# Kernel tuning notes

Measured on AMD Instinct MI355X. Metric: run time of the kernel, lower is better.

## Reference

```python
import jax, jax.numpy as jnp
import numpy as np

EPS_F = 1e-6   # epsilon_F global in original repo
GAMMA = 0.8
K = 5
BN_EPS = 1e-5
M = 128
N = 100000
E = 1600000
MY = 10

def setup_inputs() -> dict:
    key = jax.random.key(0)
    ks = jax.random.split(key, 6)
    X = jax.random.normal(ks[0], (M, N), dtype=jnp.float32)
    # xavier_uniform for F: limit = sqrt(6/(m+m))
    lim = float(np.sqrt(6.0 / (M + M)))
    F_mat = jax.random.uniform(ks[1], (M, M), dtype=jnp.float32, minval=-lim, maxval=lim)
    B = (1.0 / np.sqrt(M)) * jax.random.normal(ks[2], (MY, M), dtype=jnp.float32)
    bn_weight = jnp.ones((M,), dtype=jnp.float32)
    bn_bias = jnp.zeros((M,), dtype=jnp.float32)
    edge_val = jax.random.uniform(ks[3], (E,), dtype=jnp.float32)
    edge_row = jax.random.randint(ks[4], (E,), 0, N, dtype=jnp.int64 if jax.config.jax_enable_x64 else jnp.int32)
    edge_col = jax.random.randint(ks[5], (E,), 0, N, dtype=jnp.int64 if jax.config.jax_enable_x64 else jnp.int32)
    return {"X": X, "F_mat": F_mat, "B": B, "bn_weight": bn_weight,
            "bn_bias": bn_bias, "edge_val": edge_val,
            "edge_row": edge_row, "edge_col": edge_col}

def reference(X, F_mat, B, bn_weight, bn_bias, edge_val, edge_row, edge_col):
    n = X.shape[1]
    # normalized Gram matrix g(F) = F^T F / (||F^T F||_fro + eps)
    FF = F_mat.T @ F_mat                       # [m, m]
    G = FF / (jnp.linalg.norm(FF) + EPS_F)
    X_first = X                                # [m, n]

    def step(Xc, _):
        Y = Xc.T                               # [n, m]
        # SpMM: (S_t @ Y)[r] += val * Y[c]
        SY = jax.ops.segment_sum(edge_val[:, None] * Y[edge_col], edge_row,
                                 num_segments=n)   # [n, m]
        Xn = GAMMA * (G @ SY.T) + X_first          # [m, n]
        return Xn, None

    Xk, _ = jax.lax.scan(step, X, None, length=K)
    out = Xk.T                                 # [n, m]
    # BatchNorm1d over feature dim (training-mode batch stats); dropout omitted (eval)
    mu = out.mean(axis=0)
    var = out.var(axis=0)
    out = (out - mu) * jax.lax.rsqrt(var + BN_EPS) * bn_weight + bn_bias
    return out @ B.T                           # [n, m_y]
```

## Files before the change

kernel.cpp:

```cpp
#include <hip/hip_runtime.h>
#include <math.h>

#define MDIM 128
#define MY 10
#define GAMMA 0.8f
#define KITER 5

__device__ __forceinline__ float bf2f(unsigned short h) {
    return __uint_as_float(((unsigned int)h) << 16);
}
__device__ __forceinline__ unsigned short f2bf(float f) {
    unsigned int u = __float_as_uint(f);
    u += 0x7fffu + ((u >> 16) & 1u);
    return (unsigned short)(u >> 16);
}

__global__ void k_transpose(const float* __restrict__ X, float* __restrict__ Y0,
                            unsigned short* __restrict__ Y0h, int n) {
    __shared__ float tile[32][33];
    int r0 = blockIdx.x * 32;
    int f0 = blockIdx.y * 32;
    int tx = threadIdx.x, ty = threadIdx.y;
    #pragma unroll
    for (int i = 0; i < 32; i += 8) {
        tile[ty + i][tx] = X[(size_t)(f0 + ty + i) * n + (r0 + tx)];
    }
    __syncthreads();
    #pragma unroll
    for (int i = 0; i < 32; i += 8) {
        float v = tile[tx][ty + i];
        Y0[(size_t)(r0 + ty + i) * MDIM + (f0 + tx)] = v;
        Y0h[(size_t)(r0 + ty + i) * MDIM + (f0 + tx)] = f2bf(v);
    }
}

__global__ void k_gram(const float* __restrict__ F, float* __restrict__ FF,
                       float* __restrict__ normAcc) {
    int i = blockIdx.x, j = threadIdx.x;
    float acc = 0.f;
    for (int k = 0; k < MDIM; ++k)
        acc = fmaf(F[k * MDIM + i], F[k * MDIM + j], acc);
    FF[i * MDIM + j] = acc;
    __shared__ float red[MDIM];
    red[j] = acc * acc;
    __syncthreads();
    for (int s = 64; s > 0; s >>= 1) {
        if (j < s) red[j] += red[j + s];
        __syncthreads();
    }
    if (j == 0) atomicAdd(normAcc, red[0]);
}

__global__ void k_gnorm(const float* __restrict__ FF, const float* __restrict__ normAcc,
                        float* __restrict__ G) {
    int idx = blockIdx.x * 256 + threadIdx.x;
    float s = GAMMA / (sqrtf(*normAcc) + 1e-6f);
    G[idx] = FF[idx] * s;
}

__global__ void k_hist(const int* __restrict__ erow, int* __restrict__ cnt, int E) {
    int e = blockIdx.x * 256 + threadIdx.x;
    if (e < E) atomicAdd(&cnt[erow[e]], 1);
}

__global__ void k_scan1(const int* __restrict__ cnt, int* __restrict__ blockSums, int n) {
    int tid = threadIdx.x;
    int base = blockIdx.x * 1024 + tid * 4;
    int s = 0;
    if (base + 3 < n) {
        int4 v = *(const int4*)&cnt[base];
        s = v.x + v.y + v.z + v.w;
    } else {
        for (int i = 0; i < 4; ++i)
            if (base + i < n) s += cnt[base + i];
    }
    __shared__ int red[256];
    red[tid] = s;
    __syncthreads();
    for (int st = 128; st > 0; st >>= 1) {
        if (tid < st) red[tid] += red[tid + st];
        __syncthreads();
    }
    if (tid == 0) blockSums[blockIdx.x] = red[0];
}

__global__ void k_scan2(int* __restrict__ blockSums, int* __restrict__ row_off,
                        int nb, int n) {
    __shared__ int s[256];
    int tid = threadIdx.x;
    int v = (tid < nb) ? blockSums[tid] : 0;
    s[tid] = v;
    __syncthreads();
    for (int off = 1; off < 256; off <<= 1) {
        int t = (tid >= off) ? s[tid - off] : 0;
        __syncthreads();
        s[tid] += t;
        __syncthreads();
    }
    if (tid < nb) blockSums[tid] = s[tid] - v;
    if (tid == 0) row_off[n] = s[255];
}

__global__ void k_scan3(const int* __restrict__ cnt, const int* __restrict__ blockOff,
                        int* __restrict__ row_off, int n) {
    int tid = threadIdx.x;
    int base = blockIdx.x * 1024 + tid * 4;
    int v[4];
    #pragma unroll
    for (int i = 0; i < 4; ++i) v[i] = (base + i < n) ? cnt[base + i] : 0;
    int local = v[0] + v[1] + v[2] + v[3];
    __shared__ int s[256];
    s[tid] = local;
    __syncthreads();
    for (int off = 1; off < 256; off <<= 1) {
        int t = (tid >= off) ? s[tid - off] : 0;
        __syncthreads();
        s[tid] += t;
        __syncthreads();
    }
    int excl = s[tid] - local + blockOff[blockIdx.x];
    #pragma unroll
    for (int i = 0; i < 4; ++i) {
        if (base + i < n) { row_off[base + i] = excl; excl += v[i]; }
    }
}

__global__ void k_scatter(const int* __restrict__ erow, const int* __restrict__ ecol,
                          const float* __restrict__ eval_, int* __restrict__ cursor,
                          int* __restrict__ csr_col, float* __restrict__ csr_val, int E) {
    int e = blockIdx.x * 256 + threadIdx.x;
    if (e < E) {
        int r = erow[e];
        int pos = atomicAdd(&cursor[r], 1);
        csr_col[pos] = ecol[e];
        csr_val[pos] = eval_[e];
    }
}

__global__ void __launch_bounds__(256) k_spmm(const unsigned short* __restrict__ Yh,
                                              const int* __restrict__ row_off,
                                              const int* __restrict__ csr_col,
                                              const float* __restrict__ csr_val,
                                              float* __restrict__ SY, int n) {
    int row = blockIdx.x * 8 + (threadIdx.x >> 5);
    int tx = threadIdx.x & 31;
    if (row >= n) return;
    int e0 = row_off[row], e1 = row_off[row + 1];
    float4 acc = make_float4(0.f, 0.f, 0.f, 0.f);
    int e = e0;
    for (; e + 4 <= e1; e += 4) {
        float v0 = csr_val[e + 0];
        float v1 = csr_val[e + 1];
        float v2 = csr_val[e + 2];
        float v3 = csr_val[e + 3];
        int c0 = csr_col[e + 0];
        int c1 = csr_col[e + 1];
        int c2 = csr_col[e + 2];
        int c3 = csr_col[e + 3];
        ushort4 h0 = *(const ushort4*)&Yh[(size_t)c0 * MDIM + tx * 4];
        ushort4 h1 = *(const ushort4*)&Yh[(size_t)c1 * MDIM + tx * 4];
        ushort4 h2 = *(const ushort4*)&Yh[(size_t)c2 * MDIM + tx * 4];
        ushort4 h3 = *(const ushort4*)&Yh[(size_t)c3 * MDIM + tx * 4];
        acc.x = fmaf(v0, bf2f(h0.x), acc.x);
        acc.y = fmaf(v0, bf2f(h0.y), acc.y);
        acc.z = fmaf(v0, bf2f(h0.z), acc.z);
        acc.w = fmaf(v0, bf2f(h0.w), acc.w);
        acc.x = fmaf(v1, bf2f(h1.x), acc.x);
        acc.y = fmaf(v1, bf2f(h1.y), acc.y);
        acc.z = fmaf(v1, bf2f(h1.z), acc.z);
        acc.w = fmaf(v1, bf2f(h1.w), acc.w);
        acc.x = fmaf(v2, bf2f(h2.x), acc.x);
        acc.y = fmaf(v2, bf2f(h2.y), acc.y);
        acc.z = fmaf(v2, bf2f(h2.z), acc.z);
        acc.w = fmaf(v2, bf2f(h2.w), acc.w);
        acc.x = fmaf(v3, bf2f(h3.x), acc.x);
        acc.y = fmaf(v3, bf2f(h3.y), acc.y);
        acc.z = fmaf(v3, bf2f(h3.z), acc.z);
        acc.w = fmaf(v3, bf2f(h3.w), acc.w);
    }
    for (; e < e1; ++e) {
        float v = csr_val[e];
        int c = csr_col[e];
        ushort4 h = *(const ushort4*)&Yh[(size_t)c * MDIM + tx * 4];
        acc.x = fmaf(v, bf2f(h.x), acc.x);
        acc.y = fmaf(v, bf2f(h.y), acc.y);
        acc.z = fmaf(v, bf2f(h.z), acc.z);
        acc.w = fmaf(v, bf2f(h.w), acc.w);
    }
    *(float4*)&SY[(size_t)row * MDIM + tx * 4] = acc;
}

__global__ void __launch_bounds__(256) k_gemm(const float* __restrict__ SY,
                                              const float* __restrict__ G,
                                              const float* __restrict__ Y0,
                                              float* __restrict__ Yout,
                                              unsigned short* __restrict__ Yhout,
                                              int writeH, int n) {
    __shared__ float sG[MDIM * MDIM];
    int tid = threadIdx.x;
    #pragma unroll
    for (int i = 0; i < 16; ++i) {
        int idx = (i * 256 + tid) * 4;
        *(float4*)&sG[idx] = *(const float4*)&G[idx];
    }
    __syncthreads();
    int tx = tid & 31, ty = tid >> 5;
    size_t r0 = (size_t)blockIdx.x * 32 + ty * 4;
    int f0 = tx * 4;
    float4 acc[4];
    #pragma unroll
    for (int i = 0; i < 4; ++i) acc[i] = make_float4(0.f, 0.f, 0.f, 0.f);
    for (int j = 0; j < MDIM; j += 4) {
        float4 g0 = *(const float4*)&sG[(j + 0) * MDIM + f0];
        float4 g1 = *(const float4*)&sG[(j + 1) * MDIM + f0];
        float4 g2 = *(const float4*)&sG[(j + 2) * MDIM + f0];
        float4 g3 = *(const float4*)&sG[(j + 3) * MDIM + f0];
        #pragma unroll
        for (int i = 0; i < 4; ++i) {
            float4 sr = *(const float4*)&SY[(r0 + i) * MDIM + j];
            acc[i].x = fmaf(sr.x, g0.x, acc[i].x);
            acc[i].y = fmaf(sr.x, g0.y, acc[i].y);
            acc[i].z = fmaf(sr.x, g0.z, acc[i].z);
            acc[i].w = fmaf(sr.x, g0.w, acc[i].w);
            acc[i].x = fmaf(sr.y, g1.x, acc[i].x);
            acc[i].y = fmaf(sr.y, g1.y, acc[i].y);
            acc[i].z = fmaf(sr.y, g1.z, acc[i].z);
            acc[i].w = fmaf(sr.y, g1.w, acc[i].w);
            acc[i].x = fmaf(sr.z, g2.x, acc[i].x);
            acc[i].y = fmaf(sr.z, g2.y, acc[i].y);
            acc[i].z = fmaf(sr.z, g2.z, acc[i].z);
            acc[i].w = fmaf(sr.z, g2.w, acc[i].w);
            acc[i].x = fmaf(sr.w, g3.x, acc[i].x);
            acc[i].y = fmaf(sr.w, g3.y, acc[i].y);
            acc[i].z = fmaf(sr.w, g3.z, acc[i].z);
            acc[i].w = fmaf(sr.w, g3.w, acc[i].w);
        }
    }
    #pragma unroll
    for (int i = 0; i < 4; ++i) {
        float4 y0 = *(const float4*)&Y0[(r0 + i) * MDIM + f0];
        float4 o;
        o.x = acc[i].x + y0.x;
        o.y = acc[i].y + y0.y;
        o.z = acc[i].z + y0.z;
        o.w = acc[i].w + y0.w;
        *(float4*)&Yout[(r0 + i) * MDIM + f0] = o;
        if (writeH) {
            ushort4 h;
            h.x = f2bf(o.x);
            h.y = f2bf(o.y);
            h.z = f2bf(o.z);
            h.w = f2bf(o.w);
            *(ushort4*)&Yhout[(r0 + i) * MDIM + f0] = h;
        }
    }
}

__global__ void k_bnstats(const float* __restrict__ Y, float* __restrict__ stats, int n) {
    int f = threadIdx.x;
    int chunk = (n + gridDim.x - 1) / gridDim.x;
    int rbeg = blockIdx.x * chunk;
    int rend = rbeg + chunk;
    if (rend > n) rend = n;
    float s = 0.f, sq = 0.f;
    for (int r = rbeg; r < rend; ++r) {
        float v = Y[(size_t)r * MDIM + f];
        s += v;
        sq = fmaf(v, v, sq);
    }
    atomicAdd(&stats[f], s);
    atomicAdd(&stats[MDIM + f], sq);
}

__global__ void k_finalize(const float* __restrict__ stats, const float* __restrict__ B,
                           const float* __restrict__ bnw, const float* __restrict__ bnb,
                           float* __restrict__ Bs, float* __restrict__ cvec, int n) {
    int f = threadIdx.x;
    float inv_n = 1.f / (float)n;
    float mu = stats[f] * inv_n;
    float var = stats[MDIM + f] * inv_n - mu * mu;
    float rs = rsqrtf(var + 1e-5f);
    float sw = rs * bnw[f];
    float cv = bnb[f] - mu * sw;
    __shared__ float red[MDIM];
    for (int o = 0; o < MY; ++o) {
        float b = B[o * MDIM + f];
        Bs[o * MDIM + f] = b * sw;
        red[f] = b * cv;
        __syncthreads();
        for (int s = 64; s > 0; s >>= 1) {
            if (f < s) red[f] += red[f + s];
            __syncthreads();
        }
        if (f == 0) cvec[o] = red[0];
        __syncthreads();
    }
}

__global__ void __launch_bounds__(256) k_project(const float* __restrict__ Y,
                                                 const float* __restrict__ Bs,
                                                 const float* __restrict__ cvec,
                                                 float* __restrict__ out, int n) {
    __shared__ float yt[16 * 129];
    __shared__ float sB[MY * 129];
    __shared__ float sc[MY];
    int tid = threadIdx.x;
    size_t rbase = (size_t)blockIdx.x * 16;
    for (int idx = tid; idx < 16 * MDIM; idx += 256) {
        int r = idx >> 7, f = idx & 127;
        yt[r * 129 + f] = Y[(rbase + r) * MDIM + f];
    }
    for (int idx = tid; idx < MY * MDIM; idx += 256) {
        int o = idx >> 7, f = idx & 127;
        sB[o * 129 + f] = Bs[idx];
    }
    if (tid < MY) sc[tid] = cvec[tid];
    __syncthreads();
    if (tid < 16 * MY) {
        int r = tid / MY, o = tid % MY;
        float acc = sc[o];
        for (int f = 0; f < MDIM; ++f)
            acc = fmaf(yt[r * 129 + f], sB[o * 129 + f], acc);
        out[(rbase + r) * MY + o] = acc;
    }
}

extern "C" void kernel_launch(void* const* d_in, const int* in_sizes, int n_in,
                              void* d_out, int out_size, void* d_ws, size_t ws_size,
                              hipStream_t stream) {
    const float* X    = (const float*)d_in[0];
    const float* F    = (const float*)d_in[1];
    const float* B    = (const float*)d_in[2];
    const float* bnw  = (const float*)d_in[3];
    const float* bnb  = (const float*)d_in[4];
    const float* ev   = (const float*)d_in[5];
    const int*   erow = (const int*)d_in[6];
    const int*   ecol = (const int*)d_in[7];
    float* out = (float*)d_out;
    const int n = in_sizes[0] / MDIM;
    const int E = in_sizes[5];

    char* w = (char*)d_ws;
    size_t off = 0;
    auto carve = [&](size_t bytes) -> void* {
        void* p = w + off;
        off += (bytes + 255) & ~(size_t)255;
        return p;
    };
    float*          Y0    = (float*)carve((size_t)n * MDIM * 4);
    float*          Ycur  = (float*)carve((size_t)n * MDIM * 4);
    float*          SY    = (float*)carve((size_t)n * MDIM * 4);
    unsigned short* Yh    = (unsigned short*)carve((size_t)n * MDIM * 2);
    float* FF        = (float*)carve(MDIM * MDIM * 4);
    float* G         = (float*)carve(MDIM * MDIM * 4);
    float* csr_val   = (float*)carve((size_t)E * 4);
    int*   csr_col   = (int*)carve((size_t)E * 4);
    int*   row_off   = (int*)carve((size_t)(n + 1) * 4);
    int*   cursor    = (int*)carve((size_t)n * 4);
    int*   cnt       = (int*)carve((size_t)n * 4);
    int*   blockSums = (int*)carve(1024 * 4);
    float* normAcc   = (float*)carve(4);
    float* stats     = (float*)carve(2 * MDIM * 4);
    float* Bs        = (float*)carve(MY * MDIM * 4);
    float* cvec      = (float*)carve(MY * 4);
    (void)ws_size;

    hipMemsetAsync(cnt, 0, (size_t)n * 4, stream);
    hipMemsetAsync(normAcc, 0, 4, stream);
    hipMemsetAsync(stats, 0, 2 * MDIM * 4, stream);

    k_transpose<<<dim3(n / 32, MDIM / 32), dim3(32, 8), 0, stream>>>(X, Y0, Yh, n);
    k_gram<<<MDIM, MDIM, 0, stream>>>(F, FF, normAcc);
    k_gnorm<<<MDIM * MDIM / 256, 256, 0, stream>>>(FF, normAcc, G);

    const int nb = (n + 1023) / 1024;
    k_hist<<<(E + 255) / 256, 256, 0, stream>>>(erow, cnt, E);
    k_scan1<<<nb, 256, 0, stream>>>(cnt, blockSums, n);
    k_scan2<<<1, 256, 0, stream>>>(blockSums, row_off, nb, n);
    k_scan3<<<nb, 256, 0, stream>>>(cnt, blockSums, row_off, n);
    hipMemcpyAsync(cursor, row_off, (size_t)n * 4, hipMemcpyDeviceToDevice, stream);
    k_scatter<<<(E + 255) / 256, 256, 0, stream>>>(erow, ecol, ev, cursor, csr_col, csr_val, E);

    for (int k = 0; k < KITER; ++k) {
        k_spmm<<<(n + 7) / 8, 256, 0, stream>>>(Yh, row_off, csr_col, csr_val, SY, n);
        int writeH = (k < KITER - 1) ? 1 : 0;
        k_gemm<<<n / 32, 256, 0, stream>>>(SY, G, Y0, Ycur, Yh, writeH, n);
    }

    k_bnstats<<<256, MDIM, 0, stream>>>(Ycur, stats, n);
    k_finalize<<<1, MDIM, 0, stream>>>(stats, B, bnw, bnb, Bs, cvec, n);
    k_project<<<n / 16, 256, 0, stream>>>(Ycur, Bs, cvec, out, n);
}
```

Measured before the change: 1.118 ms.

## Fuse SpMM, G-GEMM and BN statistics into one kernel per iteration

```diff
diff --git a/kernel.cpp b/kernel.cpp
--- a/kernel.cpp
+++ b/kernel.cpp
@@ -127,115 +127,123 @@
 
 __global__ void k_scatter(const int* __restrict__ erow, const int* __restrict__ ecol,
                           const float* __restrict__ eval_, int* __restrict__ cursor,
-                          int* __restrict__ csr_col, float* __restrict__ csr_val, int E) {
+                          int2* __restrict__ csr_cv, int E) {
     int e = blockIdx.x * 256 + threadIdx.x;
     if (e < E) {
         int r = erow[e];
         int pos = atomicAdd(&cursor[r], 1);
-        csr_col[pos] = ecol[e];
-        csr_val[pos] = eval_[e];
-    }
-}
-
-__global__ void __launch_bounds__(256) k_spmm(const unsigned short* __restrict__ Yh,
-                                              const int* __restrict__ row_off,
-                                              const int* __restrict__ csr_col,
-                                              const float* __restrict__ csr_val,
-                                              float* __restrict__ SY, int n) {
-    int row = blockIdx.x * 8 + (threadIdx.x >> 5);
-    int tx = threadIdx.x & 31;
-    if (row >= n) return;
-    int e0 = row_off[row], e1 = row_off[row + 1];
-    float4 acc = make_float4(0.f, 0.f, 0.f, 0.f);
-    int e = e0;
-    for (; e + 4 <= e1; e += 4) {
-        float v0 = csr_val[e + 0];
-        float v1 = csr_val[e + 1];
-        float v2 = csr_val[e + 2];
-        float v3 = csr_val[e + 3];
-        int c0 = csr_col[e + 0];
-        int c1 = csr_col[e + 1];
-        int c2 = csr_col[e + 2];
-        int c3 = csr_col[e + 3];
-        ushort4 h0 = *(const ushort4*)&Yh[(size_t)c0 * MDIM + tx * 4];
-        ushort4 h1 = *(const ushort4*)&Yh[(size_t)c1 * MDIM + tx * 4];
-        ushort4 h2 = *(const ushort4*)&Yh[(size_t)c2 * MDIM + tx * 4];
-        ushort4 h3 = *(const ushort4*)&Yh[(size_t)c3 * MDIM + tx * 4];
-        acc.x = fmaf(v0, bf2f(h0.x), acc.x);
-        acc.y = fmaf(v0, bf2f(h0.y), acc.y);
-        acc.z = fmaf(v0, bf2f(h0.z), acc.z);
-        acc.w = fmaf(v0, bf2f(h0.w), acc.w);
-        acc.x = fmaf(v1, bf2f(h1.x), acc.x);
-        acc.y = fmaf(v1, bf2f(h1.y), acc.y);
-        acc.z = fmaf(v1, bf2f(h1.z), acc.z);
-        acc.w = fmaf(v1, bf2f(h1.w), acc.w);
-        acc.x = fmaf(v2, bf2f(h2.x), acc.x);
-        acc.y = fmaf(v2, bf2f(h2.y), acc.y);
-        acc.z = fmaf(v2, bf2f(h2.z), acc.z);
-        acc.w = fmaf(v2, bf2f(h2.w), acc.w);
-        acc.x = fmaf(v3, bf2f(h3.x), acc.x);
-        acc.y = fmaf(v3, bf2f(h3.y), acc.y);
-        acc.z = fmaf(v3, bf2f(h3.z), acc.z);
-        acc.w = fmaf(v3, bf2f(h3.w), acc.w);
-    }
-    for (; e < e1; ++e) {
-        float v = csr_val[e];
-        int c = csr_col[e];
-        ushort4 h = *(const ushort4*)&Yh[(size_t)c * MDIM + tx * 4];
-        acc.x = fmaf(v, bf2f(h.x), acc.x);
-        acc.y = fmaf(v, bf2f(h.y), acc.y);
-        acc.z = fmaf(v, bf2f(h.z), acc.z);
-        acc.w = fmaf(v, bf2f(h.w), acc.w);
-    }
-    *(float4*)&SY[(size_t)row * MDIM + tx * 4] = acc;
-}
-
-__global__ void __launch_bounds__(256) k_gemm(const float* __restrict__ SY,
-                                              const float* __restrict__ G,
-                                              const float* __restrict__ Y0,
-                                              float* __restrict__ Yout,
-                                              unsigned short* __restrict__ Yhout,
-                                              int writeH, int n) {
-    __shared__ float sG[MDIM * MDIM];
+        csr_cv[pos] = make_int2(ecol[e], __float_as_int(eval_[e]));
+    }
+}
+
+__global__ void __launch_bounds__(256) k_fused(const unsigned short* __restrict__ Yh,
+                                               const int* __restrict__ row_off,
+                                               const int2* __restrict__ csr_cv,
+                                               const float* __restrict__ G,
+                                               const float* __restrict__ Y0,
+                                               float* __restrict__ Yout,
+                                               unsigned short* __restrict__ Yhout,
+                                               float* __restrict__ stats,
+                                               int writeH, int writeF, int n) {
+    __shared__ float sGt[32 * MDIM];
+    __shared__ float sSY[32 * MDIM];
     int tid = threadIdx.x;
-    #pragma unroll
-    for (int i = 0; i < 16; ++i) {
-        int idx = (i * 256 + tid) * 4;
-        *(float4*)&sG[idx] = *(const float4*)&G[idx];
-    }
-    __syncthreads();
-    int tx = tid & 31, ty = tid >> 5;
-    size_t r0 = (size_t)blockIdx.x * 32 + ty * 4;
+    int ty = tid >> 5;
+    int tx = tid & 31;
+    int rbase = blockIdx.x * 32;
+
+    for (int i = 0; i < 4; ++i) {
+        int rloc = ty * 4 + i;
+        int e0 = row_off[rbase + rloc];
+        int e1 = row_off[rbase + rloc + 1];
+        float4 a = make_float4(0.f, 0.f, 0.f, 0.f);
+        int e = e0;
+        for (; e + 4 <= e1; e += 4) {
+            int2 p0 = csr_cv[e + 0];
+            int2 p1 = csr_cv[e + 1];
+            int2 p2 = csr_cv[e + 2];
+            int2 p3 = csr_cv[e + 3];
+            ushort4 h0 = *(const ushort4*)&Yh[(size_t)p0.x * MDIM + tx * 4];
+            ushort4 h1 = *(const ushort4*)&Yh[(size_t)p1.x * MDIM + tx * 4];
+            ushort4 h2 = *(const ushort4*)&Yh[(size_t)p2.x * MDIM + tx * 4];
+            ushort4 h3 = *(const ushort4*)&Yh[(size_t)p3.x * MDIM + tx * 4];
+            float v0 = __int_as_float(p0.y);
+            float v1 = __int_as_float(p1.y);
+            float v2 = __int_as_float(p2.y);
+            float v3 = __int_as_float(p3.y);
+            a.x = fmaf(v0, bf2f(h0.x), a.x);
+            a.y = fmaf(v0, bf2f(h0.y), a.y);
+            a.z = fmaf(v0, bf2f(h0.z), a.z);
+            a.w = fmaf(v0, bf2f(h0.w), a.w);
+            a.x = fmaf(v1, bf2f(h1.x), a.x);
+            a.y = fmaf(v1, bf2f(h1.y), a.y);
+            a.z = fmaf(v1, bf2f(h1.z), a.z);
+            a.w = fmaf(v1, bf2f(h1.w), a.w);
+            a.x = fmaf(v2, bf2f(h2.x), a.x);
+            a.y = fmaf(v2, bf2f(h2.y), a.y);
+            a.z = fmaf(v2, bf2f(h2.z), a.z);
+            a.w = fmaf(v2, bf2f(h2.w), a.w);
+            a.x = fmaf(v3, bf2f(h3.x), a.x);
+            a.y = fmaf(v3, bf2f(h3.y), a.y);
+            a.z = fmaf(v3, bf2f(h3.z), a.z);
+            a.w = fmaf(v3, bf2f(h3.w), a.w);
+        }
+        for (; e < e1; ++e) {
+            int2 p = csr_cv[e];
+            float v = __int_as_float(p.y);
+            ushort4 h = *(const ushort4*)&Yh[(size_t)p.x * MDIM + tx * 4];
+            a.x = fmaf(v, bf2f(h.x), a.x);
+            a.y = fmaf(v, bf2f(h.y), a.y);
+            a.z = fmaf(v, bf2f(h.z), a.z);
+            a.w = fmaf(v, bf2f(h.w), a.w);
+        }
+        *(float4*)&sSY[rloc * MDIM + tx * 4] = a;
+    }
+
+    size_t r0 = (size_t)rbase + ty * 4;
     int f0 = tx * 4;
     float4 acc[4];
     #pragma unroll
     for (int i = 0; i < 4; ++i) acc[i] = make_float4(0.f, 0.f, 0.f, 0.f);
-    for (int j = 0; j < MDIM; j += 4) {
-        float4 g0 = *(const float4*)&sG[(j + 0) * MDIM + f0];
-        float4 g1 = *(const float4*)&sG[(j + 1) * MDIM + f0];
-        float4 g2 = *(const float4*)&sG[(j + 2) * MDIM + f0];
-        float4 g3 = *(const float4*)&sG[(j + 3) * MDIM + f0];
+
+    for (int jt = 0; jt < MDIM; jt += 32) {
+        if (jt) __syncthreads();
         #pragma unroll
         for (int i = 0; i < 4; ++i) {
-            float4 sr = *(const float4*)&SY[(r0 + i) * MDIM + j];
-            acc[i].x = fmaf(sr.x, g0.x, acc[i].x);
-            acc[i].y = fmaf(sr.x, g0.y, acc[i].y);
-            acc[i].z = fmaf(sr.x, g0.z, acc[i].z);
-            acc[i].w = fmaf(sr.x, g0.w, acc[i].w);
-            acc[i].x = fmaf(sr.y, g1.x, acc[i].x);
-            acc[i].y = fmaf(sr.y, g1.y, acc[i].y);
-            acc[i].z = fmaf(sr.y, g1.z, acc[i].z);
-            acc[i].w = fmaf(sr.y, g1.w, acc[i].w);
-            acc[i].x = fmaf(sr.z, g2.x, acc[i].x);
-            acc[i].y = fmaf(sr.z, g2.y, acc[i].y);
-            acc[i].z = fmaf(sr.z, g2.z, acc[i].z);
-            acc[i].w = fmaf(sr.z, g2.w, acc[i].w);
-            acc[i].x = fmaf(sr.w, g3.x, acc[i].x);
-            acc[i].y = fmaf(sr.w, g3.y, acc[i].y);
-            acc[i].z = fmaf(sr.w, g3.z, acc[i].z);
-            acc[i].w = fmaf(sr.w, g3.w, acc[i].w);
-        }
-    }
+            int idx = (i * 256 + tid) * 4;
+            *(float4*)&sGt[idx] = *(const float4*)&G[jt * MDIM + idx];
+        }
+        __syncthreads();
+        for (int j = 0; j < 32; j += 4) {
+            float4 g0 = *(const float4*)&sGt[(j + 0) * MDIM + f0];
+            float4 g1 = *(const float4*)&sGt[(j + 1) * MDIM + f0];
+            float4 g2 = *(const float4*)&sGt[(j + 2) * MDIM + f0];
+            float4 g3 = *(const float4*)&sGt[(j + 3) * MDIM + f0];
+            #pragma unroll
+            for (int i = 0; i < 4; ++i) {
+                float4 sr = *(const float4*)&sSY[(ty * 4 + i) * MDIM + jt + j];
+                acc[i].x = fmaf(sr.x, g0.x, acc[i].x);
+                acc[i].y = fmaf(sr.x, g0.y, acc[i].y);
+                acc[i].z = fmaf(sr.x, g0.z, acc[i].z);
+                acc[i].w = fmaf(sr.x, g0.w, acc[i].w);
+                acc[i].x = fmaf(sr.y, g1.x, acc[i].x);
+                acc[i].y = fmaf(sr.y, g1.y, acc[i].y);
+                acc[i].z = fmaf(sr.y, g1.z, acc[i].z);
+                acc[i].w = fmaf(sr.y, g1.w, acc[i].w);
+                acc[i].x = fmaf(sr.z, g2.x, acc[i].x);
+                acc[i].y = fmaf(sr.z, g2.y, acc[i].y);
+                acc[i].z = fmaf(sr.z, g2.z, acc[i].z);
+                acc[i].w = fmaf(sr.z, g2.w, acc[i].w);
+                acc[i].x = fmaf(sr.w, g3.x, acc[i].x);
+                acc[i].y = fmaf(sr.w, g3.y, acc[i].y);
+                acc[i].z = fmaf(sr.w, g3.z, acc[i].z);
+                acc[i].w = fmaf(sr.w, g3.w, acc[i].w);
+            }
+        }
+    }
+
+    float4 bs = make_float4(0.f, 0.f, 0.f, 0.f);
+    float4 bq = make_float4(0.f, 0.f, 0.f, 0.f);
     #pragma unroll
     for (int i = 0; i < 4; ++i) {
         float4 y0 = *(const float4*)&Y0[(r0 + i) * MDIM + f0];
@@ -244,7 +252,14 @@
         o.y = acc[i].y + y0.y;
         o.z = acc[i].z + y0.z;
         o.w = acc[i].w + y0.w;
-        *(float4*)&Yout[(r0 + i) * MDIM + f0] = o;
+        if (writeF) {
+            *(float4*)&Yout[(r0 + i) * MDIM + f0] = o;
+            bs.x += o.x; bs.y += o.y; bs.z += o.z; bs.w += o.w;
+            bq.x = fmaf(o.x, o.x, bq.x);
+            bq.y = fmaf(o.y, o.y, bq.y);
+            bq.z = fmaf(o.z, o.z, bq.z);
+            bq.w = fmaf(o.w, o.w, bq.w);
+        }
         if (writeH) {
             ushort4 h;
             h.x = f2bf(o.x);
@@ -254,22 +269,23 @@
             *(ushort4*)&Yhout[(r0 + i) * MDIM + f0] = h;
         }
     }
-}
-
-__global__ void k_bnstats(const float* __restrict__ Y, float* __restrict__ stats, int n) {
-    int f = threadIdx.x;
-    int chunk = (n + gridDim.x - 1) / gridDim.x;
-    int rbeg = blockIdx.x * chunk;
-    int rend = rbeg + chunk;
-    if (rend > n) rend = n;
-    float s = 0.f, sq = 0.f;
-    for (int r = rbeg; r < rend; ++r) {
-        float v = Y[(size_t)r * MDIM + f];
-        s += v;
-        sq = fmaf(v, v, sq);
-    }
-    atomicAdd(&stats[f], s);
-    atomicAdd(&stats[MDIM + f], sq);
+
+    if (writeF) {
+        __syncthreads();
+        *(float4*)&sSY[ty * MDIM + f0] = bs;
+        *(float4*)&sSY[8 * MDIM + ty * MDIM + f0] = bq;
+        __syncthreads();
+        if (tid < MDIM) {
+            float a = 0.f, b = 0.f;
+            #pragma unroll
+            for (int t = 0; t < 8; ++t) {
+                a += sSY[t * MDIM + tid];
+                b += sSY[8 * MDIM + t * MDIM + tid];
+            }
+            atomicAdd(&stats[tid], a);
+            atomicAdd(&stats[MDIM + tid], b);
+        }
+    }
 }
 
 __global__ void k_finalize(const float* __restrict__ stats, const float* __restrict__ B,
@@ -349,12 +365,11 @@
     };
     float*          Y0    = (float*)carve((size_t)n * MDIM * 4);
     float*          Ycur  = (float*)carve((size_t)n * MDIM * 4);
-    float*          SY    = (float*)carve((size_t)n * MDIM * 4);
-    unsigned short* Yh    = (unsigned short*)carve((size_t)n * MDIM * 2);
+    unsigned short* Yh_a  = (unsigned short*)carve((size_t)n * MDIM * 2);
+    unsigned short* Yh_b  = (unsigned short*)carve((size_t)n * MDIM * 2);
     float* FF        = (float*)carve(MDIM * MDIM * 4);
     float* G         = (float*)carve(MDIM * MDIM * 4);
-    float* csr_val   = (float*)carve((size_t)E * 4);
-    int*   csr_col   = (int*)carve((size_t)E * 4);
+    int2*  csr_cv    = (int2*)carve((size_t)E * 8);
     int*   row_off   = (int*)carve((size_t)(n + 1) * 4);
     int*   cursor    = (int*)carve((size_t)n * 4);
     int*   cnt       = (int*)carve((size_t)n * 4);
@@ -369,7 +384,7 @@
     hipMemsetAsync(normAcc, 0, 4, stream);
     hipMemsetAsync(stats, 0, 2 * MDIM * 4, stream);
 
-    k_transpose<<<dim3(n / 32, MDIM / 32), dim3(32, 8), 0, stream>>>(X, Y0, Yh, n);
+    k_transpose<<<dim3(n / 32, MDIM / 32), dim3(32, 8), 0, stream>>>(X, Y0, Yh_a, n);
     k_gram<<<MDIM, MDIM, 0, stream>>>(F, FF, normAcc);
     k_gnorm<<<MDIM * MDIM / 256, 256, 0, stream>>>(FF, normAcc, G);
 
@@ -379,15 +394,17 @@
     k_scan2<<<1, 256, 0, stream>>>(blockSums, row_off, nb, n);
     k_scan3<<<nb, 256, 0, stream>>>(cnt, blockSums, row_off, n);
     hipMemcpyAsync(cursor, row_off, (size_t)n * 4, hipMemcpyDeviceToDevice, stream);
-    k_scatter<<<(E + 255) / 256, 256, 0, stream>>>(erow, ecol, ev, cursor, csr_col, csr_val, E);
+    k_scatter<<<(E + 255) / 256, 256, 0, stream>>>(erow, ecol, ev, cursor, csr_cv, E);
 
     for (int k = 0; k < KITER; ++k) {
-        k_spmm<<<(n + 7) / 8, 256, 0, stream>>>(Yh, row_off, csr_col, csr_val, SY, n);
+        const unsigned short* hin = (k & 1) ? Yh_b : Yh_a;
+        unsigned short*       hout = (k & 1) ? Yh_a : Yh_b;
         int writeH = (k < KITER - 1) ? 1 : 0;
-        k_gemm<<<n / 32, 256, 0, stream>>>(SY, G, Y0, Ycur, Yh, writeH, n);
-    }
-
-    k_bnstats<<<256, MDIM, 0, stream>>>(Ycur, stats, n);
+        int writeF = (k == KITER - 1) ? 1 : 0;
+        k_fused<<<n / 32, 256, 0, stream>>>(hin, row_off, csr_cv, G, Y0, Ycur, hout,
+                                            stats, writeH, writeF, n);
+    }
+
     k_finalize<<<1, MDIM, 0, stream>>>(stats, B, bnw, bnb, Bs, cvec, n);
     k_project<<<n / 16, 256, 0, stream>>>(Ycur, Bs, cvec, out, n);
 }
```

After: 967.8 us. 13.5% less time.
